# Kernel tuning notes

Measured on AMD Instinct MI355X. Metric: run time of the kernel, lower is better.

## Reference

```python
import jax, jax.numpy as jnp
import numpy as np

# BiDiGemma (Aveygo/SRNext) wrapping RecurrentGemma-style ResidualBlocks:
#   block0 = RECURRENT (causal conv width 4 + RG-LRU linear recurrence)
#   block1 = local (sliding-window, MQA) ATTENTION with partial RoPE
# Dropout(0.1) is treated as eval-mode identity.

B, S, D, H = 4, 4096, 256, 4
HD = D // H            # head dim = 64
E = 3 * D              # mlp_expanded_width = expand_ratio * dim
W_ATT = D              # attention_window_size = dim = 256 (divides S)
TW = 4                 # recurrentgemma temporal conv width
_NEG = -2.3819763e38   # recurrentgemma masking constant

_PNAMES = ["ln_gamma","ln_beta","proj_w","proj_b","fconv_w","fconv_b","bconv_w","bconv_b",
 "rn0_t","rn0_c","ly_w","ly_b","lx_w","lx_b","lo_w","lo_b","c1d_w","c1d_b",
 "a_param","ig_w","ig_b","ag_w","ag_b","mlp0_up_w","mlp0_up_b","mlp0_dn_w","mlp0_dn_b",
 "rn1_t","rn1_c","q_w","k_w","v_w","o_w","o_b","mlp1_up_w","mlp1_up_b","mlp1_dn_w","mlp1_dn_b"]


def _init_params(key):
    ks = iter(jax.random.split(key, 24))
    nrm = lambda shape, s: jax.random.normal(next(ks), shape, jnp.float32) * s
    p = {}
    p["ln_gamma"] = jnp.ones((D,), jnp.float32); p["ln_beta"] = jnp.zeros((D,), jnp.float32)
    p["proj_w"] = nrm((D, D), D ** -0.5);  p["proj_b"] = jnp.zeros((D,), jnp.float32)
    p["fconv_w"] = nrm((D, D), D ** -0.5); p["fconv_b"] = jnp.zeros((D,), jnp.float32)
    p["bconv_w"] = nrm((D, D), D ** -0.5); p["bconv_b"] = jnp.zeros((D,), jnp.float32)
    p["rn0_t"] = jnp.zeros((D,), jnp.float32); p["rn0_c"] = jnp.zeros((D,), jnp.float32)
    p["ly_w"] = nrm((D, D), D ** -0.5); p["ly_b"] = jnp.zeros((D,), jnp.float32)
    p["lx_w"] = nrm((D, D), D ** -0.5); p["lx_b"] = jnp.zeros((D,), jnp.float32)
    p["lo_w"] = nrm((D, D), D ** -0.5); p["lo_b"] = jnp.zeros((D,), jnp.float32)
    p["c1d_w"] = nrm((TW, D), 0.1);     p["c1d_b"] = jnp.zeros((D,), jnp.float32)
    p["a_param"] = jnp.log(jnp.expm1(jnp.linspace(0.9, 1.5, D, dtype=jnp.float32)))
    p["ig_w"] = nrm((H, HD, HD), HD ** -0.5); p["ig_b"] = jnp.zeros((H, HD), jnp.float32)
    p["ag_w"] = nrm((H, HD, HD), HD ** -0.5); p["ag_b"] = jnp.zeros((H, HD), jnp.float32)
    p["mlp0_up_w"] = nrm((2, D, E), D ** -0.5); p["mlp0_up_b"] = jnp.zeros((2, E), jnp.float32)
    p["mlp0_dn_w"] = nrm((E, D), E ** -0.5);    p["mlp0_dn_b"] = jnp.zeros((D,), jnp.float32)
    p["rn1_t"] = jnp.zeros((D,), jnp.float32); p["rn1_c"] = jnp.zeros((D,), jnp.float32)
    p["q_w"] = nrm((D, D), D ** -0.5); p["k_w"] = nrm((D, HD), D ** -0.5); p["v_w"] = nrm((D, HD), D ** -0.5)
    p["o_w"] = nrm((D, D), D ** -0.5); p["o_b"] = jnp.zeros((D,), jnp.float32)
    p["mlp1_up_w"] = nrm((2, D, E), D ** -0.5); p["mlp1_up_b"] = jnp.zeros((2, E), jnp.float32)
    p["mlp1_dn_w"] = nrm((E, D), E ** -0.5);    p["mlp1_dn_b"] = jnp.zeros((D,), jnp.float32)
    return p


def _gelu(x):
    return jax.nn.gelu(x, approximate=False)  # torch F.gelu default (erf)


def _rms_norm(x, scale, eps=1e-6):
    var = jnp.mean(jnp.square(x), axis=-1, keepdims=True)
    return x * jax.lax.rsqrt(var + eps) * (1.0 + scale)


def _layer_norm(x, g, b, eps=1e-5):
    m = jnp.mean(x, axis=-1, keepdims=True)
    v = jnp.mean(jnp.square(x - m), axis=-1, keepdims=True)
    return (x - m) * jax.lax.rsqrt(v + eps) * g + b


def _block_diag(x, w, b):
    # BlockDiagonalLinear: per-head [HD x HD] blocks
    xh = x.reshape(*x.shape[:-1], H, HD)
    y = jnp.einsum('bshd,hdk->bshk', xh, w) + b
    return y.reshape(*x.shape)


def _causal_conv1d(x, w, b):
    # depthwise causal conv, w: [TW, D], w[TW-1] multiplies current token
    xp = jnp.pad(x, ((0, 0), (TW - 1, 0), (0, 0)))
    out = sum(xp[:, i:i + x.shape[1], :] * w[i] for i in range(TW))
    return out + b


def _rg_lru(x, pos, a_param, ig_w, ig_b, ag_w, ag_b):
    gate_x = jax.nn.sigmoid(_block_diag(x, ig_w, ig_b))
    gate_a = jax.nn.sigmoid(_block_diag(x, ag_w, ag_b))
    log_a = -8.0 * gate_a * jax.nn.softplus(a_param)   # c = 8
    a = jnp.exp(log_a)
    mult = jnp.sqrt(-jnp.expm1(2.0 * log_a))           # sqrt(1 - a^2)
    reset = (pos == 0)[..., None]
    mult = jnp.where(reset, 1.0, mult)
    bterm = x * gate_x * mult
    def comb(e1, e2):
        a1, b1 = e1
        a2, b2 = e2
        return a1 * a2, a2 * b1 + b2
    _, h = jax.lax.associative_scan(comb, (a, bterm), axis=1)
    return h


def _rope(x, pos):
    # partial RoPE: applied to first half of head dim (recurrentgemma)
    rot, rest = jnp.split(x, 2, axis=-1)
    f = rot.shape[-1] // 2
    inv_freq = 10000.0 ** (-(2.0 / rot.shape[-1]) * jnp.arange(f, dtype=jnp.float32))
    t = pos[..., None, None].astype(jnp.float32) * inv_freq  # [b, s, 1, f]
    sin, cos = jnp.sin(t), jnp.cos(t)
    x1, x2 = jnp.split(rot, 2, axis=-1)
    return jnp.concatenate([x1 * cos - x2 * sin, x2 * cos + x1 * sin, rest], axis=-1)


def _local_attention(x, pos, q_w, k_w, v_w, o_w, o_b):
    # MQA sliding-window attention, window = W_ATT; chunked to honor locality
    b, s, _ = x.shape
    q = (x @ q_w).reshape(b, s, H, HD)
    k = (x @ k_w).reshape(b, s, 1, HD)
    v = (x @ v_w).reshape(b, s, HD)
    q = _rope(q, pos) * (HD ** -0.5)
    k = _rope(k, pos)[:, :, 0]
    Wn = W_ATT
    nb = s // Wn
    qc = q.reshape(b, nb, Wn, H, HD)
    kp = jnp.pad(k, ((0, 0), (Wn, 0), (0, 0))).reshape(b, nb + 1, Wn, HD)
    vp = jnp.pad(v, ((0, 0), (Wn, 0), (0, 0))).reshape(b, nb + 1, Wn, HD)
    kc = jnp.concatenate([kp[:, :-1], kp[:, 1:]], axis=2)  # [b, nb, 2W, HD]
    vc = jnp.concatenate([vp[:, :-1], vp[:, 1:]], axis=2)
    logits = jnp.einsum('bnqhd,bnkd->bnhqk', qc, kc)
    i = jnp.arange(Wn)[:, None]
    j = jnp.arange(2 * Wn)[None, :]
    diff = (i + Wn) - j                       # q_pos - k_pos
    base = (diff >= 0) & (diff <= Wn)         # causal & q <= k + window_size
    cidx = jnp.arange(nb)[:, None, None]
    mask = base[None] & ((cidx > 0) | (j[None] >= Wn))  # no left padding in chunk 0
    logits = jnp.where(mask[None, :, None], logits, _NEG)
    probs = jax.nn.softmax(logits, axis=-1)
    out = jnp.einsum('bnhqk,bnkd->bnqhd', probs, vc).reshape(b, s, D)
    return out @ o_w + o_b


def _mlp(x, up_w, up_b, dn_w, dn_b):
    up = jnp.einsum('bsd,cde->cbse', x, up_w) + up_b[:, None, None, :]
    act = _gelu(up[0]) * up[1]
    return act @ dn_w + dn_b


def _gemma_block(x, pos, p):
    # ResidualBlock 0: RECURRENT
    raw = x
    xn = _rms_norm(raw, p['rn0_t'])
    y = _gelu(xn @ p['ly_w'] + p['ly_b'])
    xr = xn @ p['lx_w'] + p['lx_b']
    xr = _causal_conv1d(xr, p['c1d_w'], p['c1d_b'])
    xr = _rg_lru(xr, pos, p['a_param'], p['ig_w'], p['ig_b'], p['ag_w'], p['ag_b'])
    xr = (xr * y) @ p['lo_w'] + p['lo_b']
    residual = xr + raw
    x = _rms_norm(residual, p['rn0_c'])
    x = _mlp(x, p['mlp0_up_w'], p['mlp0_up_b'], p['mlp0_dn_w'], p['mlp0_dn_b']) + residual
    # ResidualBlock 1: local ATTENTION
    raw = x
    xn = _rms_norm(raw, p['rn1_t'])
    xa = _local_attention(xn, pos, p['q_w'], p['k_w'], p['v_w'], p['o_w'], p['o_b'])
    residual = xa + raw
    x = _rms_norm(residual, p['rn1_c'])
    x = _mlp(x, p['mlp1_up_w'], p['mlp1_up_b'], p['mlp1_dn_w'], p['mlp1_dn_b']) + residual
    return x


def _forward(skip, *params):
    p = dict(zip(_PNAMES, params))
    b, s, _ = skip.shape
    pos = jnp.broadcast_to(jnp.arange(s, dtype=jnp.int32)[None], (b, s))
    x = _layer_norm(skip, p['ln_gamma'], p['ln_beta']) @ p['proj_w'] + p['proj_b']
    z = jax.nn.sigmoid(jnp.mean(jax.nn.silu(skip), axis=-1, keepdims=True))
    fwd = _gemma_block(x @ p['fconv_w'] + p['fconv_b'], pos, p)  # Conv1d k=1 == pointwise
    bwd = _gemma_block(x @ p['bconv_w'] + p['bconv_b'], pos, p)
    return z * (fwd + bwd) + skip


def setup_inputs() -> dict:
    key = jax.random.key(0)
    kx, kp = jax.random.split(key)
    inp = {"skip": jax.random.normal(kx, (B, S, D), jnp.float32)}
    inp.update(_init_params(kp))
    return inp


def reference(skip, ln_gamma, ln_beta, proj_w, proj_b, fconv_w, fconv_b, bconv_w, bconv_b, rn0_t, rn0_c, ly_w, ly_b, lx_w, lx_b, lo_w, lo_b, c1d_w, c1d_b, a_param, ig_w, ig_b, ag_w, ag_b, mlp0_up_w, mlp0_up_b, mlp0_dn_w, mlp0_dn_b, rn1_t, rn1_c, q_w, k_w, v_w, o_w, o_b, mlp1_up_w, mlp1_up_b, mlp1_dn_w, mlp1_dn_b):
    return _forward(skip, ln_gamma, ln_beta, proj_w, proj_b, fconv_w, fconv_b, bconv_w, bconv_b, rn0_t, rn0_c, ly_w, ly_b, lx_w, lx_b, lo_w, lo_b, c1d_w, c1d_b, a_param, ig_w, ig_b, ag_w, ag_b, mlp0_up_w, mlp0_up_b, mlp0_dn_w, mlp0_dn_b, rn1_t, rn1_c, q_w, k_w, v_w, o_w, o_b, mlp1_up_w, mlp1_up_b, mlp1_dn_w, mlp1_dn_b)
```

## Files before the change

kernel.cpp:

```cpp
#include <hip/hip_runtime.h>
#include <math.h>
#include <stddef.h>


#define BB   4
#define SS   4096
#define DD   256
#define HH   4
#define HDIM 64
#define EE   768
#define RR   (BB*SS)
#define RR2  (2*RR)
#define WNN  256
#define CH   64
#define NCH  (SS/CH)

typedef __attribute__((ext_vector_type(8))) short bfrag;
typedef __attribute__((ext_vector_type(4))) float f4acc;

__device__ __forceinline__ float geluf(float x){
  float u = 1.5957691216f*(x + 0.044715f*x*x*x);
  float e = __expf(u);
  float t = 1.f - 2.f/(e+1.f);
  return 0.5f*x*(1.f+t);
}
__device__ __forceinline__ float sigm(float x){ return 1.0f/(1.0f+expf(-x)); }

__device__ __forceinline__ unsigned short f2bf(float x){
  unsigned u = __float_as_uint(x);
  return (unsigned short)((u + 0x7FFFu + ((u>>16)&1u)) >> 16);
}
__device__ __forceinline__ float bf2f(unsigned short h){
  return __uint_as_float(((unsigned)h) << 16);
}
__device__ __forceinline__ void split2(float v, unsigned short* h, unsigned short* l){
  unsigned short hb = f2bf(v);
  *h = hb; *l = f2bf(v - bf2f(hb));
}

__device__ __forceinline__ float wredSum(float v){
#pragma unroll
  for(int o=32;o>0;o>>=1) v += __shfl_xor(v,o,64);
  return v;
}

__global__ __launch_bounds__(256) void ln_z_k(const float* __restrict__ skip,
    const float* __restrict__ g, const float* __restrict__ b,
    unsigned short* __restrict__ oh, unsigned short* __restrict__ ol,
    float* __restrict__ z)
{
  int row  = blockIdx.x*4 + (threadIdx.x>>6);
  int lane = threadIdx.x & 63;
  float4 v = ((const float4*)(skip + (size_t)row*DD))[lane];
  float s  = v.x+v.y+v.z+v.w;
  float sq = v.x*v.x+v.y*v.y+v.z*v.z+v.w*v.w;
  float si = v.x*sigm(v.x)+v.y*sigm(v.y)+v.z*sigm(v.z)+v.w*sigm(v.w);
  s = wredSum(s); sq = wredSum(sq); si = wredSum(si);
  float mean = s*(1.0f/DD);
  float var  = sq*(1.0f/DD) - mean*mean;
  float inv  = rsqrtf(var + 1e-5f);
  float4 gv = ((const float4*)g)[lane];
  float4 bv = ((const float4*)b)[lane];
  float o0 = (v.x-mean)*inv*gv.x + bv.x;
  float o1 = (v.y-mean)*inv*gv.y + bv.y;
  float o2 = (v.z-mean)*inv*gv.z + bv.z;
  float o3 = (v.w-mean)*inv*gv.w + bv.w;
  ushort4 hi, lo;
  split2(o0,&hi.x,&lo.x); split2(o1,&hi.y,&lo.y);
  split2(o2,&hi.z,&lo.z); split2(o3,&hi.w,&lo.w);
  ((ushort4*)(oh + (size_t)row*DD))[lane] = hi;
  ((ushort4*)(ol + (size_t)row*DD))[lane] = lo;
  if(lane==0) z[row] = sigm(si*(1.0f/DD));
}

__global__ __launch_bounds__(256) void rms_k(const float* __restrict__ x,
    const float* __restrict__ t,
    unsigned short* __restrict__ oh, unsigned short* __restrict__ ol)
{
  int row  = blockIdx.x*4 + (threadIdx.x>>6);
  int lane = threadIdx.x & 63;
  float4 v = ((const float4*)(x + (size_t)row*DD))[lane];
  float sq = v.x*v.x+v.y*v.y+v.z*v.z+v.w*v.w;
  sq = wredSum(sq);
  float inv = rsqrtf(sq*(1.0f/DD) + 1e-6f);
  float4 tv = ((const float4*)t)[lane];
  float o0 = v.x*inv*(1.0f+tv.x);
  float o1 = v.y*inv*(1.0f+tv.y);
  float o2 = v.z*inv*(1.0f+tv.z);
  float o3 = v.w*inv*(1.0f+tv.w);
  ushort4 hi, lo;
  split2(o0,&hi.x,&lo.x); split2(o1,&hi.y,&lo.y);
  split2(o2,&hi.z,&lo.z); split2(o3,&hi.w,&lo.w);
  ((ushort4*)(oh + (size_t)row*DD))[lane] = hi;
  ((ushort4*)(ol + (size_t)row*DD))[lane] = lo;
}

struct TS  { const float* s; unsigned short* h; unsigned short* l; int K; int N; };
struct TS8 { TS t[8]; };

__global__ __launch_bounds__(256) void tsplit8_k(TS8 g){
  TS tt = g.t[blockIdx.y];
  int idx = blockIdx.x*256 + threadIdx.x;
  int tot = tt.K*tt.N;
  if(idx >= tot) return;
  int k = idx / tt.N;
  int n = idx - k*tt.N;
  float x = tt.s[idx];
  unsigned short hb = f2bf(x);
  unsigned short lb = f2bf(x - bf2f(hb));
  tt.h[(size_t)n*tt.K + k] = hb;
  tt.l[(size_t)n*tt.K + k] = lb;
}

template<int BN, int MODE, int DUAL, int OUT, int TERMS>
__global__ __launch_bounds__(256) void gemm_mfma(
    const unsigned short* __restrict__ Ah_g, const unsigned short* __restrict__ Al_g,
    const unsigned short* __restrict__ B0h, const unsigned short* __restrict__ B0l,
    const unsigned short* __restrict__ B1h, const unsigned short* __restrict__ B1l,
    const float* __restrict__ bias0, const float* __restrict__ bias1,
    const float* __restrict__ Res, float* __restrict__ C,
    unsigned short* __restrict__ Ch, unsigned short* __restrict__ Cl,
    int K, int lda, int ldc)
{
  constexpr int NT = BN/32;
  constexpr int ST = 40;
  __shared__ unsigned short Ash[128*ST];
  __shared__ unsigned short Asl[TERMS==3 ? 128*ST : 8];
  __shared__ unsigned short Bsh[BN*ST];
  __shared__ unsigned short Bsl[TERMS>=2 ? BN*ST : 8];
  __shared__ unsigned short B2h[DUAL?BN*ST:8];
  __shared__ unsigned short B2l[(DUAL && TERMS>=2)?BN*ST:8];

  const int tid  = threadIdx.x;
  const int lane = tid & 63, wave = tid >> 6;
  const int wm = wave >> 1, wn = wave & 1;
  const int bm = blockIdx.y*128, bn = blockIdx.x*BN;
  const int m16 = lane & 15, q = lane >> 4;

  f4acc acc[4][NT];
  f4acc acc2[DUAL?4:1][DUAL?NT:1];
#pragma unroll
  for(int i=0;i<4;i++)
#pragma unroll
    for(int j=0;j<NT;j++){
      acc[i][j] = (f4acc)0.f;
      if constexpr(DUAL) acc2[i][j] = (f4acc)0.f;
    }

  const int r0 = tid >> 2, c0 = tid & 3;
  const int coff = c0*8;
  const int d0 = r0*ST + coff, d1 = (r0+64)*ST + coff;

  const unsigned short* pAh0 = Ah_g + (size_t)(bm+r0)*lda + coff;
  const unsigned short* pAh1 = pAh0 + (size_t)64*lda;
  const unsigned short* pAl0 = (TERMS==3) ? (Al_g + (size_t)(bm+r0)*lda + coff)
                                          : (const unsigned short*)nullptr;
  const unsigned short* pAl1 = (TERMS==3) ? (pAl0 + (size_t)64*lda)
                                          : (const unsigned short*)nullptr;
  const unsigned short *pB0h0=nullptr,*pB0h1=nullptr,*pB0l0=nullptr,*pB0l1=nullptr;
  const unsigned short *pBa=nullptr,*pBb=nullptr,*pBc=nullptr,*pBd=nullptr;
  if constexpr(BN==128){
    pB0h0 = B0h + (size_t)(bn+r0)*K + coff;  pB0h1 = pB0h0 + (size_t)64*K;
    if constexpr(TERMS>=2){
      pB0l0 = B0l + (size_t)(bn+r0)*K + coff;  pB0l1 = pB0l0 + (size_t)64*K;
    }
  } else {
    pBa = B0h + (size_t)(bn+r0)*K + coff;
    if constexpr(TERMS>=2) pBb = B0l + (size_t)(bn+r0)*K + coff;
    if constexpr(DUAL){
      pBc = B1h + (size_t)(bn+r0)*K + coff;
      if constexpr(TERMS>=2) pBd = B1l + (size_t)(bn+r0)*K + coff;
    }
  }

  for(int k0 = 0; k0 < K; k0 += 32){
    *(float4*)&Ash[d0] = *(const float4*)(pAh0 + k0);
    *(float4*)&Ash[d1] = *(const float4*)(pAh1 + k0);
    if constexpr(TERMS==3){
      *(float4*)&Asl[d0] = *(const float4*)(pAl0 + k0);
      *(float4*)&Asl[d1] = *(const float4*)(pAl1 + k0);
    }
    if constexpr(BN==128){
      *(float4*)&Bsh[d0] = *(const float4*)(pB0h0 + k0);
      *(float4*)&Bsh[d1] = *(const float4*)(pB0h1 + k0);
      if constexpr(TERMS>=2){
        *(float4*)&Bsl[d0] = *(const float4*)(pB0l0 + k0);
        *(float4*)&Bsl[d1] = *(const float4*)(pB0l1 + k0);
      }
    } else {
      *(float4*)&Bsh[d0] = *(const float4*)(pBa + k0);
      if constexpr(TERMS>=2) *(float4*)&Bsl[d0] = *(const float4*)(pBb + k0);
      if constexpr(DUAL){
        *(float4*)&B2h[d0] = *(const float4*)(pBc + k0);
        if constexpr(TERMS>=2) *(float4*)&B2l[d0] = *(const float4*)(pBd + k0);
      }
    }
    __syncthreads();

    bfrag ah[4], al[TERMS==3?4:1], b0hf[NT], b0lf[TERMS>=2?NT:1];
    bfrag b1hf[DUAL?NT:1], b1lf[(DUAL&&TERMS>=2)?NT:1];
#pragma unroll
    for(int mi=0;mi<4;mi++){
      int row = wm*64 + mi*16 + m16;
      ah[mi] = *(const bfrag*)&Ash[row*ST + q*8];
      if constexpr(TERMS==3) al[mi] = *(const bfrag*)&Asl[row*ST + q*8];
    }
#pragma unroll
    for(int ni=0;ni<NT;ni++){
      int n = wn*(BN/2) + ni*16 + m16;
      b0hf[ni] = *(const bfrag*)&Bsh[n*ST + q*8];
      if constexpr(TERMS>=2) b0lf[ni] = *(const bfrag*)&Bsl[n*ST + q*8];
      if constexpr(DUAL){
        b1hf[ni] = *(const bfrag*)&B2h[n*ST + q*8];
        if constexpr(TERMS>=2) b1lf[ni] = *(const bfrag*)&B2l[n*ST + q*8];
      }
    }
#pragma unroll
    for(int mi=0;mi<4;mi++)
#pragma unroll
      for(int ni=0;ni<NT;ni++){
        acc[mi][ni] = __builtin_amdgcn_mfma_f32_16x16x32_bf16(ah[mi], b0hf[ni], acc[mi][ni],0,0,0);
        if constexpr(TERMS>=2)
          acc[mi][ni] = __builtin_amdgcn_mfma_f32_16x16x32_bf16(ah[mi], b0lf[ni], acc[mi][ni],0,0,0);
        if constexpr(TERMS==3)
          acc[mi][ni] = __builtin_amdgcn_mfma_f32_16x16x32_bf16(al[mi], b0hf[ni], acc[mi][ni],0,0,0);
        if constexpr(DUAL){
          acc2[mi][ni] = __builtin_amdgcn_mfma_f32_16x16x32_bf16(ah[mi], b1hf[ni], acc2[mi][ni],0,0,0);
          if constexpr(TERMS>=2)
            acc2[mi][ni] = __builtin_amdgcn_mfma_f32_16x16x32_bf16(ah[mi], b1lf[ni], acc2[mi][ni],0,0,0);
          if constexpr(TERMS==3)
            acc2[mi][ni] = __builtin_amdgcn_mfma_f32_16x16x32_bf16(al[mi], b1hf[ni], acc2[mi][ni],0,0,0);
        }
      }
    __syncthreads();
  }

  if constexpr(OUT==0 || OUT==1 || OUT==5){
#pragma unroll
    for(int ni=0;ni<NT;ni++){
      const int col = bn + wn*(BN/2) + ni*16 + m16;
      float bv0 = (MODE&1) ? bias0[col] : 0.f;
      float bv1 = DUAL ? bias1[col] : 0.f;
#pragma unroll
      for(int mi=0;mi<4;mi++){
#pragma unroll
        for(int r=0;r<4;r++){
          const int row = bm + wm*64 + mi*16 + q*4 + r;
          float v = acc[mi][ni][r] + bv0;
          if constexpr(DUAL){
            float v2 = acc2[mi][ni][r] + bv1;
            v = geluf(v) * v2;
          } else if(MODE&2){
            v = geluf(v);
          }
          if(MODE&8) v += Res[(size_t)row*ldc + col];
          if constexpr(OUT==0){
            C[(size_t)row*ldc + col] = v;
          } else if constexpr(OUT==1){
            unsigned short hb = f2bf(v);
            Ch[(size_t)row*ldc + col] = hb;
            Cl[(size_t)row*ldc + col] = f2bf(v - bf2f(hb));
          } else {
            Ch[(size_t)row*ldc + col] = f2bf(v);
          }
        }
      }
    }
  } else if constexpr(OUT==2){
    const int hb = bn + wn*64;
    const float p = (float)m16;
    const float invf = __expf(-p * 0.575646273248511f);
#pragma unroll
    for(int mi=0;mi<4;mi++){
#pragma unroll
      for(int r=0;r<4;r++){
        const int row = bm + wm*64 + mi*16 + q*4 + r;
        const int s = row & (SS-1);
        float t = (float)s * invf;
        float sn, cs; __sincosf(t, &sn, &cs);
        float x1 = acc[mi][0][r], x2 = acc[mi][1][r];
        float v0 = (x1*cs - x2*sn)*0.125f;
        float v1 = (x2*cs + x1*sn)*0.125f;
        float v2 = acc[mi][2][r]*0.125f;
        float v3 = acc[mi][3][r]*0.125f;
        size_t base = (size_t)row*ldc + hb;
        unsigned short hh;
        hh=f2bf(v0); Ch[base+m16]=hh;    Cl[base+m16]   =f2bf(v0-bf2f(hh));
        hh=f2bf(v1); Ch[base+16+m16]=hh; Cl[base+16+m16]=f2bf(v1-bf2f(hh));
        hh=f2bf(v2); Ch[base+32+m16]=hh; Cl[base+32+m16]=f2bf(v2-bf2f(hh));
        hh=f2bf(v3); Ch[base+48+m16]=hh; Cl[base+48+m16]=f2bf(v3-bf2f(hh));
      }
    }
  } else if constexpr(OUT==3){
    const float p = (float)m16;
    const float invf = __expf(-p * 0.575646273248511f);
#pragma unroll
    for(int mi=0;mi<4;mi++){
#pragma unroll
      for(int r=0;r<4;r++){
        const int row = bm + wm*64 + mi*16 + q*4 + r;
        const int s = row & (SS-1);
        float v0, v1;
        if(wn==0){
          float t = (float)s * invf;
          float sn, cs; __sincosf(t, &sn, &cs);
          float x1 = acc[mi][0][r], x2 = acc[mi][1][r];
          v0 = x1*cs - x2*sn;
          v1 = x2*cs + x1*sn;
        } else {
          v0 = acc[mi][0][r]; v1 = acc[mi][1][r];
        }
        size_t base = (size_t)row*ldc + wn*32;
        unsigned short hh;
        hh=f2bf(v0); Ch[base+m16]=hh;    Cl[base+m16]   =f2bf(v0-bf2f(hh));
        hh=f2bf(v1); Ch[base+16+m16]=hh; Cl[base+16+m16]=f2bf(v1-bf2f(hh));
      }
    }
  } else if constexpr(OUT==4){
#pragma unroll
    for(int ni=0;ni<NT;ni++){
      const int col = wn*32 + ni*16 + m16;
#pragma unroll
      for(int mi=0;mi<4;mi++){
        const int rowb = bm + wm*64 + mi*16 + q*4;
        const int b = rowb >> 12, sl = rowb & (SS-1);
        ushort4 hv;
        hv.x = f2bf(acc[mi][ni][0]); hv.y = f2bf(acc[mi][ni][1]);
        hv.z = f2bf(acc[mi][ni][2]); hv.w = f2bf(acc[mi][ni][3]);
        *(ushort4*)(Ch + ((size_t)(b*64 + col))*SS + sl) = hv;
      }
    }
  }
}

template<int BN, int MODE>
__global__ __launch_bounds__(256) void gemm_k(
    const float* __restrict__ A,
    const float* __restrict__ B0,
    const float* __restrict__ bias0,
    float* __restrict__ C,
    int M, int N, int K, int lda, int ldb, int ldc,
    int batA, int batB, int batC, int batBias)
{
  constexpr int BK = 16;
  constexpr int TN = BN/16;
  constexpr int NH = BN/64;
  __shared__ float Ask[BK][132];
  __shared__ float Bs [BK][BN+4];

  const int bz = blockIdx.z;
  const float* Ab  = A  + (size_t)bz*batA;
  const float* Bb  = B0 + (size_t)bz*batB;
  float* Cb = C + (size_t)bz*batC;

  const int bm = blockIdx.y*128, bn = blockIdx.x*BN;
  const int tid = threadIdx.x;
  const int tx = tid & 15, ty = tid >> 4;
  const int r0 = tid >> 2, c0 = (tid & 3)*4;
  const int br = tid >> 4;

  float acc[8][TN];
#pragma unroll
  for(int i=0;i<8;i++)
#pragma unroll
    for(int j=0;j<TN;j++) acc[i][j]=0.f;

  for(int k0=0;k0<K;k0+=BK){
#pragma unroll
    for(int hf=0;hf<2;hf++){
      float4 av = *(const float4*)(Ab + (size_t)(bm+r0+hf*64)*lda + (k0+c0));
      Ask[c0+0][r0+hf*64]=av.x; Ask[c0+1][r0+hf*64]=av.y;
      Ask[c0+2][r0+hf*64]=av.z; Ask[c0+3][r0+hf*64]=av.w;
    }
    {
      const int bc = (tid&15)*4;
      *(float4*)&Bs[br][bc] = *(const float4*)(Bb + (size_t)(k0+br)*ldb + (bn+bc));
    }
    __syncthreads();
#pragma unroll
    for(int k=0;k<BK;k++){
      float a[8];
      *(float4*)&a[0] = *(const float4*)&Ask[k][ty*8];
      *(float4*)&a[4] = *(const float4*)&Ask[k][ty*8+4];
      float bv[TN];
#pragma unroll
      for(int hh=0;hh<NH;hh++)
        *(float4*)&bv[hh*4] = *(const float4*)&Bs[k][hh*64 + tx*4];
#pragma unroll
      for(int i=0;i<8;i++)
#pragma unroll
        for(int j=0;j<TN;j++)
          acc[i][j] = fmaf(a[i], bv[j], acc[i][j]);
    }
    __syncthreads();
  }

#pragma unroll
  for(int i=0;i<8;i++){
    const int row = bm + ty*8 + i;
#pragma unroll
    for(int hh=0;hh<NH;hh++){
      const int col = bn + hh*64 + tx*4;
      float v0=acc[i][hh*4+0], v1=acc[i][hh*4+1], v2=acc[i][hh*4+2], v3=acc[i][hh*4+3];
      if(MODE&1){
        float4 bbv = *(const float4*)(bias0 + (size_t)bz*batBias + col);
        v0+=bbv.x; v1+=bbv.y; v2+=bbv.z; v3+=bbv.w;
      }
      float4 ov; ov.x=v0; ov.y=v1; ov.z=v2; ov.w=v3;
      *(float4*)(Cb + (size_t)row*ldc + col) = ov;
    }
  }
}

__global__ __launch_bounds__(256) void conv_k(const float* __restrict__ x,
    const float* __restrict__ w, const float* __restrict__ b, float* __restrict__ out)
{
  int idx = blockIdx.x*256 + threadIdx.x;
  int d = idx & (DD-1);
  int r = idx >> 8;
  int s = r & (SS-1);
  float acc = b[d];
#pragma unroll
  for(int i=0;i<4;i++){
    int t = s - 3 + i;
    if(t >= 0) acc += w[i*DD + d] * x[(size_t)(r-3+i)*DD + d];
  }
  out[idx] = acc;
}

__global__ __launch_bounds__(256) void gate_k(const float* __restrict__ x,
    float* __restrict__ ig, float* __restrict__ ag, const float* __restrict__ ap)
{
  int idx = blockIdx.x*256 + threadIdx.x;
  int d = idx & (DD-1);
  int r = idx >> 8;
  int s = r & (SS-1);
  float gx = sigm(ig[idx]);
  float ga = sigm(ag[idx]);
  float a_ = ap[d];
  float sp = (a_ > 20.f) ? a_ : log1pf(expf(a_));
  float la = -8.f * ga * sp;
  float a  = expf(la);
  float mult = (s==0) ? 1.f : sqrtf(fmaxf(-expm1f(2.f*la), 0.f));
  float bt = x[idx] * gx * mult;
  ig[idx] = a;
  ag[idx] = bt;
}

__global__ __launch_bounds__(256) void scan1_k(const float* __restrict__ A,
    const float* __restrict__ Bv, float* __restrict__ csa, float* __restrict__ csb)
{
  int idx = blockIdx.x*256 + threadIdx.x;
  int d = idx & (DD-1);
  int c = (idx >> 8) & (NCH-1);
  int b = idx >> 14;
  size_t base = ((size_t)b*SS + (size_t)c*CH)*DD + d;
  float Aa = 1.f, Bb_ = 0.f;
  for(int t=0;t<CH;t++){
    float a  = A [base + (size_t)t*DD];
    float bb = Bv[base + (size_t)t*DD];
    Aa  = a*Aa;
    Bb_ = a*Bb_ + bb;
  }
  csa[idx] = Aa; csb[idx] = Bb_;
}

__global__ __launch_bounds__(256) void scan2_k(const float* __restrict__ csa,
    float* __restrict__ csb)
{
  int idx = blockIdx.x*256 + threadIdx.x;
  int d = idx & (DD-1);
  int b = idx >> 8;
  float h = 0.f;
  for(int c=0;c<NCH;c++){
    size_t i = ((size_t)b*NCH + c)*DD + d;
    float Aa = csa[i], Bb_ = csb[i];
    csb[i] = h;
    h = Aa*h + Bb_;
  }
}

__global__ __launch_bounds__(256) void scan3_k(const float* __restrict__ A,
    const float* __restrict__ Bv, const float* __restrict__ csb,
    const unsigned short* __restrict__ Yh,
    unsigned short* __restrict__ Hh, unsigned short* __restrict__ Hl)
{
  int idx = blockIdx.x*256 + threadIdx.x;
  int d = idx & (DD-1);
  int c = (idx >> 8) & (NCH-1);
  int b = idx >> 14;
  size_t base = ((size_t)b*SS + (size_t)c*CH)*DD + d;
  float h = csb[idx];
  for(int t=0;t<CH;t++){
    float a  = A [base + (size_t)t*DD];
    float bb = Bv[base + (size_t)t*DD];
    h = a*h + bb;
    float v = h * bf2f(Yh[base + (size_t)t*DD]);
    unsigned short hb = f2bf(v);
    Hh[base + (size_t)t*DD] = hb;
    Hl[base + (size_t)t*DD] = f2bf(v - bf2f(hb));
  }
}

#define AST 72
__global__ __launch_bounds__(256) void attn_k(
    const unsigned short* __restrict__ Qh, const unsigned short* __restrict__ Ql,
    const unsigned short* __restrict__ Kh, const unsigned short* __restrict__ Kl,
    const unsigned short* __restrict__ Vt,
    unsigned short* __restrict__ Oh, unsigned short* __restrict__ Ol)
{
  __shared__ unsigned short Ksh[64*AST], Ksl[64*AST], Vsh[64*AST];
  __shared__ unsigned short Ps[4*16*AST];

  const int qt = blockIdx.x & 3, n = blockIdx.x >> 2;
  const int h = blockIdx.y, b = blockIdx.z;
  const int tid = threadIdx.x;
  const int lane = tid & 63, w = tid >> 6;
  const int m16 = lane & 15, q = lane >> 4;
  const int s0 = n*WNN + qt*64;

  const size_t qro = ((size_t)(b*SS + s0 + w*16 + m16))*DD + h*HDIM + q*8;
  bfrag qh0 = *(const bfrag*)(Qh + qro);
  bfrag qh1 = *(const bfrag*)(Qh + qro + 32);
  bfrag ql0 = *(const bfrag*)(Ql + qro);
  bfrag ql1 = *(const bfrag*)(Ql + qro + 32);

  float mrow[4], lrow[4];
  f4acc oacc[4];
#pragma unroll
  for(int i=0;i<4;i++){ mrow[i]=-3.0e38f; lrow[i]=0.f; oacc[i]=(f4acc)0.f; }

  const int ktlo = (n==0) ? 4 : qt;
  const int kthi = qt + 4;
  const int sr = tid >> 2, sc = tid & 3;

  for(int kt=ktlo; kt<=kthi; kt++){
    const int kbase = (n-1)*WNN + kt*64;
#pragma unroll
    for(int cc=0; cc<2; cc++){
      int g = sc + cc*4;
      *(float4*)&Ksh[sr*AST + g*8] =
        *(const float4*)(Kh + (size_t)(b*SS + kbase + sr)*HDIM + g*8);
      *(float4*)&Ksl[sr*AST + g*8] =
        *(const float4*)(Kl + (size_t)(b*SS + kbase + sr)*HDIM + g*8);
      *(float4*)&Vsh[sr*AST + g*8] =
        *(const float4*)(Vt + ((size_t)(b*64 + sr))*SS + kbase + g*8);
    }
    __syncthreads();

    f4acc sacc[4];
#pragma unroll
    for(int nt=0;nt<4;nt++) sacc[nt] = (f4acc)0.f;
#pragma unroll
    for(int nt=0;nt<4;nt++){
      const int kr = (nt*16+m16)*AST;
      bfrag kh0 = *(const bfrag*)&Ksh[kr + q*8];
      bfrag kh1 = *(const bfrag*)&Ksh[kr + 32 + q*8];
      bfrag kl0 = *(const bfrag*)&Ksl[kr + q*8];
      bfrag kl1 = *(const bfrag*)&Ksl[kr + 32 + q*8];
      sacc[nt] = __builtin_amdgcn_mfma_f32_16x16x32_bf16(qh0, kh0, sacc[nt],0,0,0);
      sacc[nt] = __builtin_amdgcn_mfma_f32_16x16x32_bf16(qh0, kl0, sacc[nt],0,0,0);
      sacc[nt] = __builtin_amdgcn_mfma_f32_16x16x32_bf16(ql0, kh0, sacc[nt],0,0,0);
      sacc[nt] = __builtin_amdgcn_mfma_f32_16x16x32_bf16(qh1, kh1, sacc[nt],0,0,0);
      sacc[nt] = __builtin_amdgcn_mfma_f32_16x16x32_bf16(qh1, kl1, sacc[nt],0,0,0);
      sacc[nt] = __builtin_amdgcn_mfma_f32_16x16x32_bf16(ql1, kh1, sacc[nt],0,0,0);
    }

    const bool needlo = (kt == qt+4);
    const bool needhi = (kt == qt);
#pragma unroll
    for(int r=0;r<4;r++){
      int qp = qt*64 + w*16 + q*4 + r;
      float sv[4];
      float tm = -3.0e38f;
#pragma unroll
      for(int nt=0;nt<4;nt++){
        float scv = sacc[nt][r];
        if(needlo || needhi){
          int kj = kt*64 + nt*16 + m16;
          int diff = qp + WNN - kj;
          bool ok = (!needlo || diff >= 0) && (!needhi || diff <= WNN);
          scv = ok ? scv : -3.0e38f;
        }
        sv[nt] = scv;
        tm = fmaxf(tm, scv);
      }
#pragma unroll
      for(int off=1; off<16; off<<=1) tm = fmaxf(tm, __shfl_xor(tm, off, 64));
      float mn = fmaxf(mrow[r], tm);
      float alpha = __expf(mrow[r]-mn);
      float rs = 0.f;
#pragma unroll
      for(int nt=0;nt<4;nt++){
        float pp = __expf(sv[nt]-mn);
        rs += pp;
        Ps[w*16*AST + (q*4+r)*AST + nt*16 + m16] = f2bf(pp);
      }
#pragma unroll
      for(int off=1; off<16; off<<=1) rs += __shfl_xor(rs, off, 64);
      lrow[r] = lrow[r]*alpha + rs;
      mrow[r] = mn;
#pragma unroll
      for(int nt=0;nt<4;nt++) oacc[nt][r] *= alpha;
    }

#pragma unroll
    for(int s=0;s<2;s++){
      bfrag pa = *(const bfrag*)&Ps[w*16*AST + m16*AST + s*32 + q*8];
#pragma unroll
      for(int nt=0;nt<4;nt++){
        bfrag vh_ = *(const bfrag*)&Vsh[(nt*16+m16)*AST + s*32 + q*8];
        oacc[nt] = __builtin_amdgcn_mfma_f32_16x16x32_bf16(pa, vh_, oacc[nt],0,0,0);
      }
    }
    __syncthreads();
  }

#pragma unroll
  for(int r=0;r<4;r++){
    float invl = 1.f/lrow[r];
    const size_t rowbase = ((size_t)(b*SS + s0 + w*16 + q*4 + r))*DD + h*HDIM;
#pragma unroll
    for(int nt=0;nt<4;nt++){
      float v = oacc[nt][r]*invl;
      unsigned short hb = f2bf(v);
      Oh[rowbase + nt*16 + m16] = hb;
      Ol[rowbase + nt*16 + m16] = f2bf(v - bf2f(hb));
    }
  }
}

__global__ __launch_bounds__(256) void comb_k(const float* __restrict__ of,
    const float* __restrict__ ob, const float* __restrict__ z,
    const float* __restrict__ skip, float* __restrict__ out)
{
  int idx = blockIdx.x*256 + threadIdx.x;
  int r = idx >> 8;
  out[idx] = z[r]*(of[idx]+ob[idx]) + skip[idx];
}

struct Params {
  const float *ln_gamma,*ln_beta,*proj_w,*proj_b,*fconv_w,*fconv_b,*bconv_w,*bconv_b,
    *rn0_t,*rn0_c,*ly_w,*ly_b,*lx_w,*lx_b,*lo_w,*lo_b,*c1d_w,*c1d_b,*a_param,
    *ig_w,*ig_b,*ag_w,*ag_b,*mlp0_up_w,*mlp0_up_b,*mlp0_dn_w,*mlp0_dn_b,
    *rn1_t,*rn1_c,*q_w,*k_w,*v_w,*o_w,*o_b,*mlp1_up_w,*mlp1_up_b,*mlp1_dn_w,*mlp1_dn_b;
};

struct WSplit {
  unsigned short *proj_h,*proj_l,*fconv_h,*fconv_l,*bconv_h,*bconv_l,
    *ly_h,*ly_l,*lx_h,*lx_l,*lo_h,*lo_l,*q_h,*q_l,*o_h,*o_l,
    *k_h,*k_l,*v_h,*v_l,
    *up0a_h,*up0a_l,*up0b_h,*up0b_l,*up1a_h,*up1a_l,*up1b_h,*up1b_l,
    *dn0_h,*dn0_l,*dn1_h,*dn1_l;
};

#define USN ((unsigned short*)nullptr)

extern "C" void kernel_launch(void* const* d_in, const int* in_sizes, int n_in,
                              void* d_out, int out_size, void* d_ws, size_t ws_size,
                              hipStream_t stream)
{
  (void)in_sizes; (void)n_in; (void)out_size; (void)ws_size;
  const float* skip = (const float*)d_in[0];
  Params p;
  p.ln_gamma  =(const float*)d_in[1];  p.ln_beta  =(const float*)d_in[2];
  p.proj_w    =(const float*)d_in[3];  p.proj_b   =(const float*)d_in[4];
  p.fconv_w   =(const float*)d_in[5];  p.fconv_b  =(const float*)d_in[6];
  p.bconv_w   =(const float*)d_in[7];  p.bconv_b  =(const float*)d_in[8];
  p.rn0_t     =(const float*)d_in[9];  p.rn0_c    =(const float*)d_in[10];
  p.ly_w      =(const float*)d_in[11]; p.ly_b     =(const float*)d_in[12];
  p.lx_w      =(const float*)d_in[13]; p.lx_b     =(const float*)d_in[14];
  p.lo_w      =(const float*)d_in[15]; p.lo_b     =(const float*)d_in[16];
  p.c1d_w     =(const float*)d_in[17]; p.c1d_b    =(const float*)d_in[18];
  p.a_param   =(const float*)d_in[19];
  p.ig_w      =(const float*)d_in[20]; p.ig_b     =(const float*)d_in[21];
  p.ag_w      =(const float*)d_in[22]; p.ag_b     =(const float*)d_in[23];
  p.mlp0_up_w =(const float*)d_in[24]; p.mlp0_up_b=(const float*)d_in[25];
  p.mlp0_dn_w =(const float*)d_in[26]; p.mlp0_dn_b=(const float*)d_in[27];
  p.rn1_t     =(const float*)d_in[28]; p.rn1_c    =(const float*)d_in[29];
  p.q_w       =(const float*)d_in[30]; p.k_w      =(const float*)d_in[31];
  p.v_w       =(const float*)d_in[32]; p.o_w      =(const float*)d_in[33];
  p.o_b       =(const float*)d_in[34];
  p.mlp1_up_w =(const float*)d_in[35]; p.mlp1_up_b=(const float*)d_in[36];
  p.mlp1_dn_w =(const float*)d_in[37]; p.mlp1_dn_b=(const float*)d_in[38];

  float* ws = (float*)d_ws;
  const size_t RD  = (size_t)RR*DD;
  const size_t PD2 = (size_t)RR2*DD;
  size_t off = 0;
  float* Z   = ws + off; off += 16384;
  float* XB2 = ws + off; off += 2*RD;
  float* CV2 = ws + off; off += 2*RD;
  float* W1  = ws + off; off += 2*RD;
  float* W2  = ws + off; off += 2*RD;
  float* W3  = ws + off; off += RD;
  float* W4  = ws + off; off += 2*RD;

  float* CSA = CV2;
  float* CSB = CV2 + 8*NCH*DD;

  unsigned short* NPh = (unsigned short*)W4;  unsigned short* NPl = NPh + PD2;
  unsigned short* HYh = NPh;                  unsigned short* HYl = NPl;
  unsigned short* X0h = (unsigned short*)W1;  unsigned short* X0l = X0h + (size_t)RR*DD;
  float* XR2 = W1;
  unsigned short* Qph = (unsigned short*)W1;  unsigned short* Qpl = Qph + PD2;
  float* Abuf = W2;
  unsigned short* P2h = (unsigned short*)W2;  unsigned short* P2l = P2h + PD2;
  unsigned short* Yh  = (unsigned short*)W3;
  unsigned short* KPh = (unsigned short*)W3;  unsigned short* KPl = KPh + (size_t)RR2*HDIM;
  unsigned short* Vt  = KPl + (size_t)RR2*HDIM;
  unsigned short* ACTh = (unsigned short*)W1;
  float* OUT2 = XB2;

  unsigned short* sp = (unsigned short*)(ws + off);
  WSplit w;
  auto alloc_s = [&](size_t n){ unsigned short* r = sp; sp += n; return r; };
  const size_t SDD = (size_t)DD*DD, SKV = (size_t)DD*HDIM, SUP = (size_t)DD*EE;
  w.proj_h=alloc_s(SDD);  w.proj_l=alloc_s(SDD);
  w.fconv_h=alloc_s(SDD); w.fconv_l=alloc_s(SDD);
  w.bconv_h=alloc_s(SDD); w.bconv_l=alloc_s(SDD);
  w.ly_h=alloc_s(SDD);    w.ly_l=alloc_s(SDD);
  w.lx_h=alloc_s(SDD);    w.lx_l=alloc_s(SDD);
  w.lo_h=alloc_s(SDD);    w.lo_l=alloc_s(SDD);
  w.q_h=alloc_s(SDD);     w.q_l=alloc_s(SDD);
  w.o_h=alloc_s(SDD);     w.o_l=alloc_s(SDD);
  w.k_h=alloc_s(SKV);     w.k_l=alloc_s(SKV);
  w.v_h=alloc_s(SKV);     w.v_l=alloc_s(SKV);
  w.up0a_h=alloc_s(SUP);  w.up0a_l=alloc_s(SUP);
  w.up0b_h=alloc_s(SUP);  w.up0b_l=alloc_s(SUP);
  w.up1a_h=alloc_s(SUP);  w.up1a_l=alloc_s(SUP);
  w.up1b_h=alloc_s(SUP);  w.up1b_l=alloc_s(SUP);
  w.dn0_h=alloc_s(SUP);   w.dn0_l=alloc_s(SUP);
  w.dn1_h=alloc_s(SUP);   w.dn1_l=alloc_s(SUP);

  dim3 blk(256);
  dim3 g2(2,128,1);
  dim3 g2m(2,256,1), g64m(1,256,1), gbd(1,256,4), gdual(12,256,1);

  {
    TS8 ga;
    ga.t[0] = {p.proj_w,  w.proj_h,  w.proj_l,  DD, DD};
    ga.t[1] = {p.fconv_w, w.fconv_h, w.fconv_l, DD, DD};
    ga.t[2] = {p.bconv_w, w.bconv_h, w.bconv_l, DD, DD};
    ga.t[3] = {p.ly_w,    w.ly_h,    w.ly_l,    DD, DD};
    ga.t[4] = {p.lx_w,    w.lx_h,    w.lx_l,    DD, DD};
    ga.t[5] = {p.lo_w,    w.lo_h,    w.lo_l,    DD, DD};
    ga.t[6] = {p.q_w,     w.q_h,     w.q_l,     DD, DD};
    ga.t[7] = {p.o_w,     w.o_h,     w.o_l,     DD, DD};
    tsplit8_k<<<dim3(DD*DD/256, 8), blk, 0, stream>>>(ga);
    TS8 gb;
    gb.t[0] = {p.k_w,              w.k_h,    w.k_l,    DD, HDIM};
    gb.t[1] = {p.v_w,              w.v_h,    w.v_l,    DD, HDIM};
    gb.t[2] = {p.mlp0_up_w,        w.up0a_h, w.up0a_l, DD, EE};
    gb.t[3] = {p.mlp0_up_w+(size_t)DD*EE, w.up0b_h, w.up0b_l, DD, EE};
    gb.t[4] = {p.mlp1_up_w,        w.up1a_h, w.up1a_l, DD, EE};
    gb.t[5] = {p.mlp1_up_w+(size_t)DD*EE, w.up1b_h, w.up1b_l, DD, EE};
    gb.t[6] = {p.mlp0_dn_w,        w.dn0_h,  w.dn0_l,  EE, DD};
    gb.t[7] = {p.mlp1_dn_w,        w.dn1_h,  w.dn1_l,  EE, DD};
    tsplit8_k<<<dim3(DD*EE/256, 8), blk, 0, stream>>>(gb);
  }

  ln_z_k<<<RR/4, blk, 0, stream>>>(skip, p.ln_gamma, p.ln_beta, NPh, NPl, Z);
  gemm_mfma<128,1,0,1,3><<<g2,blk,0,stream>>>(NPh,NPl, w.proj_h,w.proj_l, USN,USN,
      p.proj_b,nullptr,nullptr, nullptr, X0h, X0l, DD,DD,DD);
  gemm_mfma<128,1,0,0,3><<<g2,blk,0,stream>>>(X0h,X0l, w.fconv_h,w.fconv_l, USN,USN,
      p.fconv_b,nullptr,nullptr, XB2, USN,USN, DD,DD,DD);
  gemm_mfma<128,1,0,0,3><<<g2,blk,0,stream>>>(X0h,X0l, w.bconv_h,w.bconv_l, USN,USN,
      p.bconv_b,nullptr,nullptr, XB2 + RD, USN,USN, DD,DD,DD);

  rms_k<<<RR2/4, blk, 0, stream>>>(XB2, p.rn0_t, NPh, NPl);
  gemm_mfma<128,3,0,5,2><<<g2m,blk,0,stream>>>(NPh,USN, w.ly_h,w.ly_l, USN,USN,
      p.ly_b,nullptr,nullptr, nullptr, Yh, USN, DD,DD,DD);
  gemm_mfma<128,1,0,0,2><<<g2m,blk,0,stream>>>(NPh,USN, w.lx_h,w.lx_l, USN,USN,
      p.lx_b,nullptr,nullptr, XR2, USN,USN, DD,DD,DD);
  conv_k<<<(size_t)RR2*DD/256, blk, 0, stream>>>(XR2, p.c1d_w, p.c1d_b, CV2);
  gemm_k<64,1><<<gbd,blk,0,stream>>>(CV2,p.ig_w,p.ig_b,Abuf,
      RR2,HDIM,HDIM, DD,HDIM,DD, HDIM, HDIM*HDIM, HDIM, HDIM);
  gemm_k<64,1><<<gbd,blk,0,stream>>>(CV2,p.ag_w,p.ag_b,XR2,
      RR2,HDIM,HDIM, DD,HDIM,DD, HDIM, HDIM*HDIM, HDIM, HDIM);
  gate_k<<<(size_t)RR2*DD/256, blk, 0, stream>>>(CV2, Abuf, XR2, p.a_param);
  scan1_k<<<8*NCH*DD/256, blk,0,stream>>>(Abuf, XR2, CSA, CSB);
  scan2_k<<<8*DD/256, blk,0,stream>>>(CSA, CSB);
  scan3_k<<<8*NCH*DD/256, blk,0,stream>>>(Abuf, XR2, CSB, Yh, HYh, HYl);
  gemm_mfma<128,9,0,0,2><<<g2m,blk,0,stream>>>(HYh,USN, w.lo_h,w.lo_l, USN,USN,
      p.lo_b,nullptr, XB2, CV2, USN,USN, DD,DD,DD);
  rms_k<<<RR2/4,blk,0,stream>>>(CV2, p.rn0_c, NPh, NPl);
  gemm_mfma<64,1,1,5,1><<<gdual,blk,0,stream>>>(NPh,USN, w.up0a_h,USN,
      w.up0b_h,USN, p.mlp0_up_b, p.mlp0_up_b+EE, nullptr, nullptr,
      ACTh, USN, DD,DD,EE);
  gemm_mfma<128,9,0,0,2><<<g2m,blk,0,stream>>>(ACTh,USN, w.dn0_h,w.dn0_l, USN,USN,
      p.mlp0_dn_b,nullptr, CV2, XB2, USN,USN, EE,EE,DD);

  rms_k<<<RR2/4,blk,0,stream>>>(XB2, p.rn1_t, NPh, NPl);
  gemm_mfma<128,0,0,2,2><<<g2m,blk,0,stream>>>(NPh,USN, w.q_h,w.q_l, USN,USN,
      nullptr,nullptr,nullptr, nullptr, Qph, Qpl, DD,DD,DD);
  gemm_mfma<64,0,0,3,3><<<g64m,blk,0,stream>>>(NPh,NPl, w.k_h,w.k_l, USN,USN,
      nullptr,nullptr,nullptr, nullptr, KPh, KPl, DD,DD,HDIM);
  gemm_mfma<64,0,0,4,3><<<g64m,blk,0,stream>>>(NPh,NPl, w.v_h,w.v_l, USN,USN,
      nullptr,nullptr,nullptr, nullptr, Vt, USN, DD,DD,HDIM);
  attn_k<<<dim3(64,4,8),blk,0,stream>>>(Qph, Qpl, KPh, KPl, Vt, P2h, P2l);
  gemm_mfma<128,9,0,0,2><<<g2m,blk,0,stream>>>(P2h,USN, w.o_h,w.o_l, USN,USN,
      p.o_b,nullptr, XB2, CV2, USN,USN, DD,DD,DD);
  rms_k<<<RR2/4,blk,0,stream>>>(CV2, p.rn1_c, NPh, NPl);
  gemm_mfma<64,1,1,5,1><<<gdual,blk,0,stream>>>(NPh,USN, w.up1a_h,USN,
      w.up1b_h,USN, p.mlp1_up_b, p.mlp1_up_b+EE, nullptr, nullptr,
      ACTh, USN, DD,DD,EE);
  gemm_mfma<128,9,0,0,2><<<g2m,blk,0,stream>>>(ACTh,USN, w.dn1_h,w.dn1_l, USN,USN,
      p.mlp1_dn_b,nullptr, CV2, OUT2, USN,USN, EE,EE,DD);

  comb_k<<<RR*DD/256, blk, 0, stream>>>(OUT2, OUT2 + RD, Z, skip, (float*)d_out);
}
```

Before: 820.8 us.

## Fuse input/recurrence gate GEMMs with gate activation; prefetch K/V tiles in attention

Replaces the two block-diagonal gate GEMMs plus the separate elementwise gate kernel with one kernel. It computes both gate products from a shared A tile and applies the sigmoid/softplus/exp epilogue in registers, writing a and b directly. This removes one re-read of the conv output and the round trip of the two gate intermediates through global memory. The local-attention loop also now loads the next K/V tile into registers while the current tile is being computed, at the cost of extra register pressure.

```diff
diff --git a/kernel.cpp b/kernel.cpp
--- a/kernel.cpp
+++ b/kernel.cpp
@@ -333,82 +333,95 @@
   }
 }
 
-template<int BN, int MODE>
-__global__ __launch_bounds__(256) void gemm_k(
-    const float* __restrict__ A,
-    const float* __restrict__ B0,
-    const float* __restrict__ bias0,
-    float* __restrict__ C,
-    int M, int N, int K, int lda, int ldb, int ldc,
-    int batA, int batB, int batC, int batBias)
+__global__ __launch_bounds__(256) void gates_k(
+    const float* __restrict__ X,
+    const float* __restrict__ igw, const float* __restrict__ igb,
+    const float* __restrict__ agw, const float* __restrict__ agb,
+    const float* __restrict__ ap,
+    float* __restrict__ Aout, float* __restrict__ Bout)
 {
   constexpr int BK = 16;
-  constexpr int TN = BN/16;
-  constexpr int NH = BN/64;
   __shared__ float Ask[BK][132];
-  __shared__ float Bs [BK][BN+4];
-
-  const int bz = blockIdx.z;
-  const float* Ab  = A  + (size_t)bz*batA;
-  const float* Bb  = B0 + (size_t)bz*batB;
-  float* Cb = C + (size_t)bz*batC;
-
-  const int bm = blockIdx.y*128, bn = blockIdx.x*BN;
+  __shared__ float Bi[BK][68];
+  __shared__ float Ba[BK][68];
+
+  const int h  = blockIdx.y;
+  const int bm = blockIdx.x*128;
   const int tid = threadIdx.x;
   const int tx = tid & 15, ty = tid >> 4;
   const int r0 = tid >> 2, c0 = (tid & 3)*4;
-  const int br = tid >> 4;
-
-  float acc[8][TN];
+  const int br = tid >> 4, bc = (tid & 15)*4;
+
+  const float* Xb = X + (size_t)h*HDIM;
+  const float* wI = igw + (size_t)h*HDIM*HDIM;
+  const float* wA = agw + (size_t)h*HDIM*HDIM;
+
+  float accI[8][4], accA[8][4];
 #pragma unroll
   for(int i=0;i<8;i++)
 #pragma unroll
-    for(int j=0;j<TN;j++) acc[i][j]=0.f;
-
-  for(int k0=0;k0<K;k0+=BK){
+    for(int j=0;j<4;j++){ accI[i][j]=0.f; accA[i][j]=0.f; }
+
+  for(int k0=0;k0<HDIM;k0+=BK){
 #pragma unroll
     for(int hf=0;hf<2;hf++){
-      float4 av = *(const float4*)(Ab + (size_t)(bm+r0+hf*64)*lda + (k0+c0));
+      float4 av = *(const float4*)(Xb + (size_t)(bm+r0+hf*64)*DD + (k0+c0));
       Ask[c0+0][r0+hf*64]=av.x; Ask[c0+1][r0+hf*64]=av.y;
       Ask[c0+2][r0+hf*64]=av.z; Ask[c0+3][r0+hf*64]=av.w;
     }
-    {
-      const int bc = (tid&15)*4;
-      *(float4*)&Bs[br][bc] = *(const float4*)(Bb + (size_t)(k0+br)*ldb + (bn+bc));
-    }
+    *(float4*)&Bi[br][bc] = *(const float4*)(wI + (size_t)(k0+br)*HDIM + bc);
+    *(float4*)&Ba[br][bc] = *(const float4*)(wA + (size_t)(k0+br)*HDIM + bc);
     __syncthreads();
 #pragma unroll
     for(int k=0;k<BK;k++){
       float a[8];
       *(float4*)&a[0] = *(const float4*)&Ask[k][ty*8];
       *(float4*)&a[4] = *(const float4*)&Ask[k][ty*8+4];
-      float bv[TN];
-#pragma unroll
-      for(int hh=0;hh<NH;hh++)
-        *(float4*)&bv[hh*4] = *(const float4*)&Bs[k][hh*64 + tx*4];
+      float bi[4], ba[4];
+      *(float4*)&bi[0] = *(const float4*)&Bi[k][tx*4];
+      *(float4*)&ba[0] = *(const float4*)&Ba[k][tx*4];
 #pragma unroll
       for(int i=0;i<8;i++)
 #pragma unroll
-        for(int j=0;j<TN;j++)
-          acc[i][j] = fmaf(a[i], bv[j], acc[i][j]);
+        for(int j=0;j<4;j++){
+          accI[i][j] = fmaf(a[i], bi[j], accI[i][j]);
+          accA[i][j] = fmaf(a[i], ba[j], accA[i][j]);
+        }
     }
     __syncthreads();
   }
+
+  const int colg = h*HDIM + tx*4;
+  const float4 bI  = *(const float4*)(igb + colg);
+  const float4 bA  = *(const float4*)(agb + colg);
+  const float4 apv = *(const float4*)(ap  + colg);
+  const float* bIf = (const float*)&bI;
+  const float* bAf = (const float*)&bA;
+  const float* apf = (const float*)&apv;
+  float spv[4];
+#pragma unroll
+  for(int j=0;j<4;j++)
+    spv[j] = (apf[j] > 20.f) ? apf[j] : log1pf(expf(apf[j]));
 
 #pragma unroll
   for(int i=0;i<8;i++){
     const int row = bm + ty*8 + i;
-#pragma unroll
-    for(int hh=0;hh<NH;hh++){
-      const int col = bn + hh*64 + tx*4;
-      float v0=acc[i][hh*4+0], v1=acc[i][hh*4+1], v2=acc[i][hh*4+2], v3=acc[i][hh*4+3];
-      if(MODE&1){
-        float4 bbv = *(const float4*)(bias0 + (size_t)bz*batBias + col);
-        v0+=bbv.x; v1+=bbv.y; v2+=bbv.z; v3+=bbv.w;
-      }
-      float4 ov; ov.x=v0; ov.y=v1; ov.z=v2; ov.w=v3;
-      *(float4*)(Cb + (size_t)row*ldc + col) = ov;
-    }
+    const int s = row & (SS-1);
+    const float4 xv = *(const float4*)(X + (size_t)row*DD + colg);
+    const float* xf = (const float*)&xv;
+    float oa[4], ob[4];
+#pragma unroll
+    for(int j=0;j<4;j++){
+      float gx = sigm(accI[i][j] + bIf[j]);
+      float ga = sigm(accA[i][j] + bAf[j]);
+      float la = -8.f * ga * spv[j];
+      float a_ = expf(la);
+      float mult = (s==0) ? 1.f : sqrtf(fmaxf(-expm1f(2.f*la), 0.f));
+      oa[j] = a_;
+      ob[j] = xf[j] * gx * mult;
+    }
+    *(float4*)(Aout + (size_t)row*DD + colg) = *(const float4*)oa;
+    *(float4*)(Bout + (size_t)row*DD + colg) = *(const float4*)ob;
   }
 }
 
@@ -426,25 +439,6 @@
     if(t >= 0) acc += w[i*DD + d] * x[(size_t)(r-3+i)*DD + d];
   }
   out[idx] = acc;
-}
-
-__global__ __launch_bounds__(256) void gate_k(const float* __restrict__ x,
-    float* __restrict__ ig, float* __restrict__ ag, const float* __restrict__ ap)
-{
-  int idx = blockIdx.x*256 + threadIdx.x;
-  int d = idx & (DD-1);
-  int r = idx >> 8;
-  int s = r & (SS-1);
-  float gx = sigm(ig[idx]);
-  float ga = sigm(ag[idx]);
-  float a_ = ap[d];
-  float sp = (a_ > 20.f) ? a_ : log1pf(expf(a_));
-  float la = -8.f * ga * sp;
-  float a  = expf(la);
-  float mult = (s==0) ? 1.f : sqrtf(fmaxf(-expm1f(2.f*la), 0.f));
-  float bt = x[idx] * gx * mult;
-  ig[idx] = a;
-  ag[idx] = bt;
 }
 
 __global__ __launch_bounds__(256) void scan1_k(const float* __restrict__ A,
@@ -534,19 +528,29 @@
   const int kthi = qt + 4;
   const int sr = tid >> 2, sc = tid & 3;
 
-  for(int kt=ktlo; kt<=kthi; kt++){
+  float4 rk[2], rl[2], rv[2];
+  auto ldt = [&](int kt){
     const int kbase = (n-1)*WNN + kt*64;
 #pragma unroll
     for(int cc=0; cc<2; cc++){
       int g = sc + cc*4;
-      *(float4*)&Ksh[sr*AST + g*8] =
-        *(const float4*)(Kh + (size_t)(b*SS + kbase + sr)*HDIM + g*8);
-      *(float4*)&Ksl[sr*AST + g*8] =
-        *(const float4*)(Kl + (size_t)(b*SS + kbase + sr)*HDIM + g*8);
-      *(float4*)&Vsh[sr*AST + g*8] =
-        *(const float4*)(Vt + ((size_t)(b*64 + sr))*SS + kbase + g*8);
+      rk[cc] = *(const float4*)(Kh + (size_t)(b*SS + kbase + sr)*HDIM + g*8);
+      rl[cc] = *(const float4*)(Kl + (size_t)(b*SS + kbase + sr)*HDIM + g*8);
+      rv[cc] = *(const float4*)(Vt + ((size_t)(b*64 + sr))*SS + kbase + g*8);
+    }
+  };
+  ldt(ktlo);
+
+  for(int kt=ktlo; kt<=kthi; kt++){
+#pragma unroll
+    for(int cc=0; cc<2; cc++){
+      int g = sc + cc*4;
+      *(float4*)&Ksh[sr*AST + g*8] = rk[cc];
+      *(float4*)&Ksl[sr*AST + g*8] = rl[cc];
+      *(float4*)&Vsh[sr*AST + g*8] = rv[cc];
     }
     __syncthreads();
+    if(kt < kthi) ldt(kt+1);
 
     f4acc sacc[4];
 #pragma unroll
@@ -735,7 +739,8 @@
 
   dim3 blk(256);
   dim3 g2(2,128,1);
-  dim3 g2m(2,256,1), g64m(1,256,1), gbd(1,256,4), gdual(12,256,1);
+  dim3 g2m(2,256,1), g64m(1,256,1), gdual(12,256,1);
+  dim3 ggate(RR2/128, HH, 1);
 
   {
     TS8 ga;
@@ -774,11 +779,8 @@
   gemm_mfma<128,1,0,0,2><<<g2m,blk,0,stream>>>(NPh,USN, w.lx_h,w.lx_l, USN,USN,
       p.lx_b,nullptr,nullptr, XR2, USN,USN, DD,DD,DD);
   conv_k<<<(size_t)RR2*DD/256, blk, 0, stream>>>(XR2, p.c1d_w, p.c1d_b, CV2);
-  gemm_k<64,1><<<gbd,blk,0,stream>>>(CV2,p.ig_w,p.ig_b,Abuf,
-      RR2,HDIM,HDIM, DD,HDIM,DD, HDIM, HDIM*HDIM, HDIM, HDIM);
-  gemm_k<64,1><<<gbd,blk,0,stream>>>(CV2,p.ag_w,p.ag_b,XR2,
-      RR2,HDIM,HDIM, DD,HDIM,DD, HDIM, HDIM*HDIM, HDIM, HDIM);
-  gate_k<<<(size_t)RR2*DD/256, blk, 0, stream>>>(CV2, Abuf, XR2, p.a_param);
+  gates_k<<<ggate,blk,0,stream>>>(CV2, p.ig_w, p.ig_b, p.ag_w, p.ag_b,
+      p.a_param, Abuf, XR2);
   scan1_k<<<8*NCH*DD/256, blk,0,stream>>>(Abuf, XR2, CSA, CSB);
   scan2_k<<<8*DD/256, blk,0,stream>>>(CSA, CSB);
   scan3_k<<<8*NCH*DD/256, blk,0,stream>>>(Abuf, XR2, CSB, Yh, HYh, HYl);
```

Result: no change. 815.0 us (-0.7%).
